# Optimization experiments

Hardware: AMD Instinct MI355X
Metric: run time of the kernel (lower is better)

The kernel has to match this reference:

```python
import jax, jax.numpy as jnp
import numpy as np

TOP_K = 2  # num_experts_per_tok


def setup_inputs() -> dict:
    key = jax.random.key(0)
    k1, k2, k3, k4, k5 = jax.random.split(key, 5)
    T, H, F, E = 2048, 2048, 1024, 8
    hidden_states = jax.random.normal(k1, (T, H), dtype=jnp.float32)
    router_logits = jax.random.normal(k2, (T, E), dtype=jnp.float32)
    s = 1.0 / np.sqrt(H)
    w1 = jax.random.normal(k3, (E, H, F), dtype=jnp.float32) * s  # gate proj
    w3 = jax.random.normal(k4, (E, H, F), dtype=jnp.float32) * s  # up proj
    w2 = jax.random.normal(k5, (E, F, H), dtype=jnp.float32) * (1.0 / np.sqrt(F))  # down proj
    return {"hidden_states": hidden_states, "router_logits": router_logits,
            "w1": w1, "w3": w3, "w2": w2}


def reference(hidden_states, router_logits, w1, w3, w2):
    # Top-K routing: softmax over raw logits, take top-k probs as combine weights
    # (renormalize_topk_logits=False, routed_scaling_factor=None).
    T, E = router_logits.shape
    probs = jax.nn.softmax(router_logits.astype(jnp.float32), axis=-1)  # (T, E)
    topk_w, topk_ids = jax.lax.top_k(probs, TOP_K)                      # (T, K)
    # Scatter combine weights into a dense (T, E) matrix (zeros off top-k).
    combine = jnp.zeros((T, E), dtype=probs.dtype).at[
        jnp.arange(T)[:, None], topk_ids].add(topk_w)                    # (T, E)

    x = hidden_states
    # SwiGLU expert FFN computed per-expert (dense over all tokens, masked by
    # combine weights -> same math as fused dispatch/grouped-GEMM/combine).
    g = jnp.einsum('th,ehf->etf', x, w1)          # (E, T, F) gate
    u = jnp.einsum('th,ehf->etf', x, w3)          # (E, T, F) up
    act = jax.nn.silu(g) * u                      # (E, T, F)
    act = act * combine.T[:, :, None]             # apply combine weight pre-down-proj
    y = jnp.einsum('etf,efh->th', act, w2)        # (T, H) combined over experts
    return y.astype(hidden_states.dtype)
```

## Files before the change

### kernel.cpp

```cpp
#include <hip/hip_runtime.h>
#include <stdint.h>

#define T_TOK 2048
#define HDIM  2048
#define FDIM  1024
#define NEXP  8

#define BM   128
#define BK   64
#define NTHR 256
#define MT_MAX 16
#define BN1  64
#define BN2  128
#define NT1 (FDIM / BN1)
#define NT2 (HDIM / BN2)
#define NK1 (HDIM / BK)
#define NK2 (FDIM / BK)
#define GRID2K (NEXP * MT_MAX * NT2)
#define TILE_E 4096
#define SMEM_BYTES 36864

typedef unsigned short u16;
typedef __attribute__((ext_vector_type(16))) float f32x16;
typedef __attribute__((ext_vector_type(8))) short bf16x8;

__device__ __forceinline__ u16 f2bf(float f) {
  uint32_t u = __float_as_uint(f);
  u += 0x7FFFu + ((u >> 16) & 1u);
  return (u16)(u >> 16);
}

__device__ __forceinline__ uint32_t pack2(float lo, float hi) {
  return (uint32_t)f2bf(lo) | ((uint32_t)f2bf(hi) << 16);
}

__device__ __forceinline__ void glds16(const u16* src, u16* dst) {
  __builtin_amdgcn_global_load_lds(
      (const __attribute__((address_space(1))) uint32_t*)src,
      (__attribute__((address_space(3))) uint32_t*)dst, 16, 0, 0);
}

__global__ void route1_kernel(const float* __restrict__ logits,
                              int* __restrict__ tok_e, float* __restrict__ tok_w,
                              int* __restrict__ counts) {
  __shared__ int lcnt[NEXP];
  const int tid = threadIdx.x;
  const int t = blockIdx.x * 256 + tid;
  if (tid < NEXP) lcnt[tid] = 0;
  __syncthreads();
  float l[NEXP];
#pragma unroll
  for (int e = 0; e < NEXP; ++e) l[e] = logits[t * NEXP + e];
  float m = l[0];
#pragma unroll
  for (int e = 1; e < NEXP; ++e) m = fmaxf(m, l[e]);
  float p[NEXP]; float s = 0.f;
#pragma unroll
  for (int e = 0; e < NEXP; ++e) { p[e] = __expf(l[e] - m); s += p[e]; }
  float inv = 1.f / s;
  int i0 = 0; float p0 = p[0];
#pragma unroll
  for (int e = 1; e < NEXP; ++e) if (p[e] > p0) { p0 = p[e]; i0 = e; }
  int i1 = -1; float p1 = -1.f;
#pragma unroll
  for (int e = 0; e < NEXP; ++e) if (e != i0 && p[e] > p1) { p1 = p[e]; i1 = e; }
  tok_e[t] = i0 | (i1 << 8);
  tok_w[t * 2]     = p0 * inv;
  tok_w[t * 2 + 1] = p1 * inv;
  atomicAdd(&lcnt[i0], 1);
  atomicAdd(&lcnt[i1], 1);
  __syncthreads();
  if (tid < NEXP) atomicAdd(&counts[tid], lcnt[tid]);
}

__global__ void route2_kernel(const int* __restrict__ counts,
                              int* __restrict__ offsets, int* __restrict__ cursor) {
  if (threadIdx.x == 0) {
    int s = 0;
    for (int e = 0; e < NEXP; ++e) { offsets[e] = s; cursor[e] = s; s += counts[e]; }
    offsets[NEXP] = s;
  }
}

__global__ void route3_kernel(const int* __restrict__ tok_e, const float* __restrict__ tok_w,
                              int* __restrict__ cursor,
                              int* __restrict__ token_list, float* __restrict__ slot_w) {
  __shared__ int lcnt[NEXP], lbase[NEXP];
  const int tid = threadIdx.x;
  const int t = blockIdx.x * 256 + tid;
  if (tid < NEXP) lcnt[tid] = 0;
  __syncthreads();
  int ee = tok_e[t];
  int e0 = ee & 255, e1 = ee >> 8;
  int li0 = atomicAdd(&lcnt[e0], 1);
  int li1 = atomicAdd(&lcnt[e1], 1);
  __syncthreads();
  if (tid < NEXP) lbase[tid] = atomicAdd(&cursor[tid], lcnt[tid]);
  __syncthreads();
  int s0 = lbase[e0] + li0;
  int s1 = lbase[e1] + li1;
  token_list[s0] = t; slot_w[s0] = tok_w[t * 2];
  token_list[s1] = t; slot_w[s1] = tok_w[t * 2 + 1];
}

__device__ __forceinline__ void wconv_block(const float* __restrict__ src,
                                            u16* __restrict__ dstb,
                                            int C, int NT, int NKT,
                                            int e, int r0, int c0, uint32_t* L) {
  const int t = threadIdx.x;
  const int p  = t >> 5;
  const int ln = t & 31;
  const float* row0 = src + (size_t)(r0 + 2 * p) * C + c0;
  const float* row1 = row0 + C;
  float4 f0[8], f1[8];
#pragma unroll
  for (int j = 0; j < 8; ++j) f0[j] = *(const float4*)(row0 + j * 128 + ln * 4);
#pragma unroll
  for (int j = 0; j < 8; ++j) f1[j] = *(const float4*)(row1 + j * 128 + ln * 4);
#pragma unroll
  for (int j = 0; j < 8; ++j) {
    int n = j * 128 + ln * 4;
    L[(n + 0) * 9 + p] = pack2(f0[j].x, f1[j].x);
    L[(n + 1) * 9 + p] = pack2(f0[j].y, f1[j].y);
    L[(n + 2) * 9 + p] = pack2(f0[j].z, f1[j].z);
    L[(n + 3) * 9 + p] = pack2(f0[j].w, f1[j].w);
  }
  __syncthreads();
  const int kt = r0 >> 6, kq = (r0 >> 4) & 3;
#pragma unroll
  for (int i = 0; i < 4; ++i) {
    int n = t * 4 + i;
    const uint32_t* a = &L[n * 9];
    uint4 lo = {a[0], a[1], a[2], a[3]};
    uint4 hi = {a[4], a[5], a[6], a[7]};
    int ng = c0 + n;
    int s = (n >> 2) & 1;
    u16* tb = dstb + (((size_t)e * NT + (ng >> 6)) * NKT + kt) * TILE_E
                   + kq * 1024 + (n & 63) * 16;
    *(uint4*)(tb + s * 8)       = lo;
    *(uint4*)(tb + (s ^ 1) * 8) = hi;
  }
}

__global__ __launch_bounds__(256, 3)
void mega1_kernel(const float* __restrict__ w1, const float* __restrict__ w3,
                  u16* __restrict__ w1b, u16* __restrict__ w3b,
                  const float4* __restrict__ x, ushort4* __restrict__ xb,
                  float4* __restrict__ y4) {
  __shared__ __align__(16) uint8_t smem[SMEM_BYTES];
  const int bid = blockIdx.x;
  const int t = threadIdx.x;
  if (bid < 2048) {
    const int m = bid >> 10;
    const int r = bid & 1023;
    const int e = r >> 7;
    const int g = r & 127;
    const size_t msz = (size_t)HDIM * FDIM;
    wconv_block((m ? w3 : w1) + (size_t)e * msz, m ? w3b : w1b,
                FDIM, 16, 32, e, g * 16, 0, (uint32_t*)smem);
  } else if (bid < 2304) {
    int i = (bid - 2048) * 256 + t;
#pragma unroll
    for (int r = 0; r < 16; ++r, i += 65536) {
      float4 v = x[i];
      ushort4 o;
      o.x = f2bf(v.x); o.y = f2bf(v.y); o.z = f2bf(v.z); o.w = f2bf(v.w);
      xb[i] = o;
    }
  } else {
    int i = (bid - 2304) * 256 + t;
    float4 z = {0.f, 0.f, 0.f, 0.f};
#pragma unroll
    for (int r = 0; r < 16; ++r, i += 65536) y4[i] = z;
  }
}

__global__ __launch_bounds__(256, 3)
void mega2_kernel(const float* __restrict__ w2, u16* __restrict__ w2b,
                  const u16* __restrict__ Xb,
                  const u16* __restrict__ w1b, const u16* __restrict__ w3b,
                  const int* __restrict__ token_list,
                  const float* __restrict__ slot_w,
                  const int* __restrict__ counts,
                  const int* __restrict__ offsets,
                  u16* __restrict__ act) {
  __shared__ __align__(16) uint8_t smem[SMEM_BYTES];
  const int bid = blockIdx.x;
  if (bid < 1024) {
    const int e = bid >> 7;
    const int r = bid & 127;
    const int g = r & 63;
    const int half = r >> 6;
    wconv_block(w2 + (size_t)e * HDIM * FDIM, w2b,
                HDIM, 32, 16, e, g * 16, half * 1024, (uint32_t*)smem);
    return;
  }
  const int gb = bid - 1024;
  const int e  = gb >> 8;
  const int mt = (gb >> 4) & 15;
  const int nt = gb & 15;
  const int cnt = counts[e];
  if (mt * BM >= cnt) return;
  const int off = offsets[e];
  const int tid  = threadIdx.x;
  const int lane = tid & 63;
  const int wid  = tid >> 6;
  const int wr = wid >> 1;
  const int wc = wid & 1;

  u16* A_lds  = (u16*)smem;
  u16* B1_lds = (u16*)(smem + 16384);
  u16* B3_lds = (u16*)(smem + 24576);

  const u16* a_src[4];
#pragma unroll
  for (int i = 0; i < 4; ++i) {
    int row = (wid * 4 + i) * 8 + (lane >> 3);
    int mg = mt * BM + row;
    int mc = (mg < cnt) ? mg : (cnt - 1);
    int tok = token_list[off + mc];
    a_src[i] = Xb + (size_t)tok * HDIM + (((lane & 7) ^ (row & 7)) * 8);
  }
  const u16* b1_src[2];
  const u16* b3_src[2];
  {
    size_t tbase = ((size_t)(e * 16 + nt) * 32) * TILE_E;
#pragma unroll
    for (int i = 0; i < 2; ++i) {
      int c = wid * 2 + i;
      b1_src[i] = w1b + tbase + c * 512 + lane * 8;
      b3_src[i] = w3b + tbase + c * 512 + lane * 8;
    }
  }

  f32x16 accg[2] = {};
  f32x16 accu[2] = {};

#pragma unroll
  for (int i = 0; i < 4; ++i) glds16(a_src[i], &A_lds[(wid * 4 + i) * 512]);
#pragma unroll
  for (int i = 0; i < 2; ++i) {
    glds16(b1_src[i], &B1_lds[(wid * 2 + i) * 512]);
    glds16(b3_src[i], &B3_lds[(wid * 2 + i) * 512]);
  }

#pragma unroll 1
  for (int t = 0; t < NK1; ++t) {
    __syncthreads();
    bf16x8 af[2][4], bg[4], bu[4];
#pragma unroll
    for (int m = 0; m < 2; ++m) {
      int R = wr * 64 + m * 32 + (lane & 31);
#pragma unroll
      for (int kk = 0; kk < 4; ++kk) {
        int gl = kk * 2 + (lane >> 5);
        af[m][kk] = *(const bf16x8*)&A_lds[R * BK + ((gl ^ (R & 7)) * 8)];
      }
    }
    {
      int R = wc * 32 + (lane & 31);
      int base = R * 16 + (((lane >> 5) ^ ((R >> 2) & 1)) * 8);
#pragma unroll
      for (int kk = 0; kk < 4; ++kk) {
        bg[kk] = *(const bf16x8*)&B1_lds[base + kk * 1024];
        bu[kk] = *(const bf16x8*)&B3_lds[base + kk * 1024];
      }
    }
    __syncthreads();
    if (t + 1 < NK1) {
      const size_t ks = (size_t)(t + 1) * BK;
      const size_t kb = (size_t)(t + 1) * TILE_E;
#pragma unroll
      for (int i = 0; i < 4; ++i) glds16(a_src[i] + ks, &A_lds[(wid * 4 + i) * 512]);
#pragma unroll
      for (int i = 0; i < 2; ++i) {
        glds16(b1_src[i] + kb, &B1_lds[(wid * 2 + i) * 512]);
        glds16(b3_src[i] + kb, &B3_lds[(wid * 2 + i) * 512]);
      }
    }
#pragma unroll
    for (int m = 0; m < 2; ++m)
#pragma unroll
      for (int kk = 0; kk < 4; ++kk) {
        accg[m] = __builtin_amdgcn_mfma_f32_32x32x16_bf16(af[m][kk], bg[kk], accg[m], 0, 0, 0);
        accu[m] = __builtin_amdgcn_mfma_f32_32x32x16_bf16(af[m][kk], bu[kk], accu[m], 0, 0, 0);
      }
  }

  const int fcol = nt * BN1 + wc * 32 + (lane & 31);
#pragma unroll
  for (int m = 0; m < 2; ++m) {
    int base = mt * BM + wr * 64 + m * 32 + 4 * (lane >> 5);
#pragma unroll
    for (int reg = 0; reg < 16; ++reg) {
      int mg = base + (reg & 3) + 8 * (reg >> 2);
      if (mg < cnt) {
        int slot = off + mg;
        float wgt = slot_w[slot];
        float g = accg[m][reg];
        float u = accu[m][reg];
        float sv = g / (1.f + __expf(-g));
        act[(size_t)slot * FDIM + fcol] = f2bf(sv * u * wgt);
      }
    }
  }
}

__global__ __launch_bounds__(NTHR, 3)
void gemm2_kernel(const u16* __restrict__ act,
                  const u16* __restrict__ w2b,
                  const int* __restrict__ token_list,
                  const int* __restrict__ counts,
                  const int* __restrict__ offsets,
                  float* __restrict__ y) {
  const int bid = blockIdx.x;
  const int e  = bid >> 8;
  const int mt = (bid >> 4) & 15;
  const int nt = bid & 15;
  const int cnt = counts[e];
  if (mt * BM >= cnt) return;
  const int off = offsets[e];
  const int tid  = threadIdx.x;
  const int lane = tid & 63;
  const int wid  = tid >> 6;
  const int wr = wid >> 1;
  const int wc = wid & 1;

  __shared__ u16 A_lds[BM * BK];
  __shared__ u16 B_lds[BN2 * BK];

  const u16* a_src[4];
  const u16* b_src[4];
#pragma unroll
  for (int i = 0; i < 4; ++i) {
    int row = (wid * 4 + i) * 8 + (lane >> 3);
    int mg = mt * BM + row;
    int mc = (mg < cnt) ? mg : (cnt - 1);
    a_src[i] = act + (size_t)(off + mc) * FDIM + (((lane & 7) ^ (row & 7)) * 8);
    int c = wid * 4 + i;
    size_t tbase = ((size_t)(e * 32 + nt * 2 + (c >> 3)) * 16) * TILE_E;
    b_src[i] = w2b + tbase + (c & 7) * 512 + lane * 8;
  }

  f32x16 acc[2][2] = {};

#pragma unroll
  for (int i = 0; i < 4; ++i) {
    glds16(a_src[i], &A_lds[(wid * 4 + i) * 512]);
    glds16(b_src[i], &B_lds[(wid * 4 + i) * 512]);
  }

#pragma unroll 1
  for (int t = 0; t < NK2; ++t) {
    __syncthreads();
    bf16x8 af[2][4], bb[2][4];
#pragma unroll
    for (int m = 0; m < 2; ++m) {
      int R = wr * 64 + m * 32 + (lane & 31);
#pragma unroll
      for (int kk = 0; kk < 4; ++kk) {
        int gl = kk * 2 + (lane >> 5);
        af[m][kk] = *(const bf16x8*)&A_lds[R * BK + ((gl ^ (R & 7)) * 8)];
      }
    }
#pragma unroll
    for (int n = 0; n < 2; ++n) {
      int R = wc * 64 + n * 32 + (lane & 31);
      int base = (R >> 6) * TILE_E + (R & 63) * 16 + (((lane >> 5) ^ ((R >> 2) & 1)) * 8);
#pragma unroll
      for (int kk = 0; kk < 4; ++kk)
        bb[n][kk] = *(const bf16x8*)&B_lds[base + kk * 1024];
    }
    __syncthreads();
    if (t + 1 < NK2) {
      const size_t ks = (size_t)(t + 1) * BK;
      const size_t kb = (size_t)(t + 1) * TILE_E;
#pragma unroll
      for (int i = 0; i < 4; ++i) {
        glds16(a_src[i] + ks, &A_lds[(wid * 4 + i) * 512]);
        glds16(b_src[i] + kb, &B_lds[(wid * 4 + i) * 512]);
      }
    }
#pragma unroll
    for (int kk = 0; kk < 4; ++kk)
#pragma unroll
      for (int m = 0; m < 2; ++m)
#pragma unroll
        for (int n = 0; n < 2; ++n)
          acc[m][n] = __builtin_amdgcn_mfma_f32_32x32x16_bf16(af[m][kk], bb[n][kk], acc[m][n], 0, 0, 0);
  }

#pragma unroll
  for (int m = 0; m < 2; ++m) {
    int base = mt * BM + wr * 64 + m * 32 + 4 * (lane >> 5);
#pragma unroll
    for (int reg = 0; reg < 16; ++reg) {
      int mg = base + (reg & 3) + 8 * (reg >> 2);
      if (mg < cnt) {
        int slot = off + mg;
        int tok = token_list[slot];
#pragma unroll
        for (int n = 0; n < 2; ++n) {
          int hcol = nt * BN2 + wc * 64 + n * 32 + (lane & 31);
          unsafeAtomicAdd(y + (size_t)tok * HDIM + hcol, acc[m][n][reg]);
        }
      }
    }
  }
}

extern "C" void kernel_launch(void* const* d_in, const int* in_sizes, int n_in,
                              void* d_out, int out_size, void* d_ws, size_t ws_size,
                              hipStream_t stream) {
  (void)in_sizes; (void)n_in; (void)out_size; (void)ws_size;
  const float* hs     = (const float*)d_in[0];
  const float* logits = (const float*)d_in[1];
  const float* w1     = (const float*)d_in[2];
  const float* w3     = (const float*)d_in[3];
  const float* w2     = (const float*)d_in[4];
  float* y = (float*)d_out;

  uint8_t* ws = (uint8_t*)d_ws;
  int*   token_list = (int*)(ws);
  float* slot_w     = (float*)(ws + (16 << 10));
  int*   counts     = (int*)(ws + (32 << 10));
  int*   offsets    = (int*)(ws + (32 << 10) + 128);
  int*   cursor     = (int*)(ws + (32 << 10) + 256);
  int*   tok_e      = (int*)(ws + (33 << 10));
  float* tok_w      = (float*)(ws + (42 << 10));
  const size_t MB = 1 << 20;
  u16*   Xb  = (u16*)(ws + (64 << 10));
  u16*   act = (u16*)(ws + (64 << 10) + 8 * MB);
  u16*   w1b = (u16*)(ws + (64 << 10) + 16 * MB);
  u16*   w3b = (u16*)(ws + (64 << 10) + 48 * MB);
  u16*   w2b = (u16*)(ws + (64 << 10) + 80 * MB);

  hipMemsetAsync(counts, 0, NEXP * sizeof(int), stream);
  route1_kernel<<<T_TOK / 256, 256, 0, stream>>>(logits, tok_e, tok_w, counts);
  route2_kernel<<<1, 64, 0, stream>>>(counts, offsets, cursor);
  route3_kernel<<<T_TOK / 256, 256, 0, stream>>>(tok_e, tok_w, cursor, token_list, slot_w);
  mega1_kernel<<<2560, 256, 0, stream>>>(w1, w3, w1b, w3b,
                                         (const float4*)hs, (ushort4*)Xb, (float4*)y);
  mega2_kernel<<<3072, 256, 0, stream>>>(w2, w2b, Xb, w1b, w3b,
                                         token_list, slot_w, counts, offsets, act);
  gemm2_kernel<<<GRID2K, NTHR, 0, stream>>>(act, w2b, token_list, counts, offsets, y);
}
```

Before: 181.9 us.

## Double-buffer LDS tiles in both expert GEMM kernels

Gives the gate/up and down-projection GEMMs two LDS buffers each, so the next K tile's global-to-LDS load is issued into the other buffer while MFMAs run on the current one. This cuts each K step from two barriers to one. The cost is doubled shared memory (64 KB per block), which lowers the occupancy hint from 3 to 2 blocks per CU and reduces latency hiding across blocks.

```diff
diff --git a/kernel.cpp b/kernel.cpp
--- a/kernel.cpp
+++ b/kernel.cpp
@@ -18,7 +18,7 @@
 #define NK2 (FDIM / BK)
 #define GRID2K (NEXP * MT_MAX * NT2)
 #define TILE_E 4096
-#define SMEM_BYTES 36864
+#define SMEM2 65536
 
 typedef unsigned short u16;
 typedef __attribute__((ext_vector_type(16))) float f32x16;
@@ -147,7 +147,7 @@
                   u16* __restrict__ w1b, u16* __restrict__ w3b,
                   const float4* __restrict__ x, ushort4* __restrict__ xb,
                   float4* __restrict__ y4) {
-  __shared__ __align__(16) uint8_t smem[SMEM_BYTES];
+  __shared__ __align__(16) uint8_t smem[36864];
   const int bid = blockIdx.x;
   const int t = threadIdx.x;
   if (bid < 2048) {
@@ -175,7 +175,7 @@
   }
 }
 
-__global__ __launch_bounds__(256, 3)
+__global__ __launch_bounds__(256, 2)
 void mega2_kernel(const float* __restrict__ w2, u16* __restrict__ w2b,
                   const u16* __restrict__ Xb,
                   const u16* __restrict__ w1b, const u16* __restrict__ w3b,
@@ -184,7 +184,7 @@
                   const int* __restrict__ counts,
                   const int* __restrict__ offsets,
                   u16* __restrict__ act) {
-  __shared__ __align__(16) uint8_t smem[SMEM_BYTES];
+  __shared__ __align__(16) uint8_t smem[SMEM2];
   const int bid = blockIdx.x;
   if (bid < 1024) {
     const int e = bid >> 7;
@@ -208,9 +208,12 @@
   const int wr = wid >> 1;
   const int wc = wid & 1;
 
-  u16* A_lds  = (u16*)smem;
-  u16* B1_lds = (u16*)(smem + 16384);
-  u16* B3_lds = (u16*)(smem + 24576);
+  u16* A0  = (u16*)smem;
+  u16* A1  = (u16*)(smem + 16384);
+  u16* B10 = (u16*)(smem + 32768);
+  u16* B30 = (u16*)(smem + 40960);
+  u16* B11 = (u16*)(smem + 49152);
+  u16* B31 = (u16*)(smem + 57344);
 
   const u16* a_src[4];
 #pragma unroll
@@ -235,57 +238,63 @@
 
   f32x16 accg[2] = {};
   f32x16 accu[2] = {};
-
-#pragma unroll
-  for (int i = 0; i < 4; ++i) glds16(a_src[i], &A_lds[(wid * 4 + i) * 512]);
-#pragma unroll
-  for (int i = 0; i < 2; ++i) {
-    glds16(b1_src[i], &B1_lds[(wid * 2 + i) * 512]);
-    glds16(b3_src[i], &B3_lds[(wid * 2 + i) * 512]);
-  }
+  bf16x8 af[2][4], bg[4], bu[4];
+
+#define STAGE1(Ab, B1b, B3b, T)                                          \
+  { const size_t ks = (size_t)(T) * BK;                                  \
+    const size_t kb = (size_t)(T) * TILE_E;                              \
+    _Pragma("unroll")                                                    \
+    for (int i = 0; i < 4; ++i) glds16(a_src[i] + ks, &Ab[(wid * 4 + i) * 512]); \
+    _Pragma("unroll")                                                    \
+    for (int i = 0; i < 2; ++i) {                                        \
+      glds16(b1_src[i] + kb, &B1b[(wid * 2 + i) * 512]);                 \
+      glds16(b3_src[i] + kb, &B3b[(wid * 2 + i) * 512]);                 \
+    } }
+
+#define FRAGS1(Ab, B1b, B3b)                                             \
+  { _Pragma("unroll")                                                    \
+    for (int m = 0; m < 2; ++m) {                                        \
+      int R = wr * 64 + m * 32 + (lane & 31);                            \
+      _Pragma("unroll")                                                  \
+      for (int kk = 0; kk < 4; ++kk) {                                   \
+        int gl = kk * 2 + (lane >> 5);                                   \
+        af[m][kk] = *(const bf16x8*)&Ab[R * BK + ((gl ^ (R & 7)) * 8)];  \
+      }                                                                  \
+    }                                                                    \
+    { int R = wc * 32 + (lane & 31);                                     \
+      int base = R * 16 + (((lane >> 5) ^ ((R >> 2) & 1)) * 8);          \
+      _Pragma("unroll")                                                  \
+      for (int kk = 0; kk < 4; ++kk) {                                   \
+        bg[kk] = *(const bf16x8*)&B1b[base + kk * 1024];                 \
+        bu[kk] = *(const bf16x8*)&B3b[base + kk * 1024];                 \
+      } } }
+
+#define MFMA1                                                            \
+  { _Pragma("unroll")                                                    \
+    for (int m = 0; m < 2; ++m)                                          \
+      _Pragma("unroll")                                                  \
+      for (int kk = 0; kk < 4; ++kk) {                                   \
+        accg[m] = __builtin_amdgcn_mfma_f32_32x32x16_bf16(af[m][kk], bg[kk], accg[m], 0, 0, 0); \
+        accu[m] = __builtin_amdgcn_mfma_f32_32x32x16_bf16(af[m][kk], bu[kk], accu[m], 0, 0, 0); \
+      } }
+
+  STAGE1(A0, B10, B30, 0);
+  __syncthreads();
 
 #pragma unroll 1
-  for (int t = 0; t < NK1; ++t) {
+  for (int t = 0; t < NK1; t += 2) {
+    FRAGS1(A0, B10, B30);
+    STAGE1(A1, B11, B31, t + 1);
+    MFMA1;
     __syncthreads();
-    bf16x8 af[2][4], bg[4], bu[4];
-#pragma unroll
-    for (int m = 0; m < 2; ++m) {
-      int R = wr * 64 + m * 32 + (lane & 31);
-#pragma unroll
-      for (int kk = 0; kk < 4; ++kk) {
-        int gl = kk * 2 + (lane >> 5);
-        af[m][kk] = *(const bf16x8*)&A_lds[R * BK + ((gl ^ (R & 7)) * 8)];
-      }
-    }
-    {
-      int R = wc * 32 + (lane & 31);
-      int base = R * 16 + (((lane >> 5) ^ ((R >> 2) & 1)) * 8);
-#pragma unroll
-      for (int kk = 0; kk < 4; ++kk) {
-        bg[kk] = *(const bf16x8*)&B1_lds[base + kk * 1024];
-        bu[kk] = *(const bf16x8*)&B3_lds[base + kk * 1024];
-      }
-    }
+    FRAGS1(A1, B11, B31);
+    if (t + 2 < NK1) STAGE1(A0, B10, B30, t + 2);
+    MFMA1;
     __syncthreads();
-    if (t + 1 < NK1) {
-      const size_t ks = (size_t)(t + 1) * BK;
-      const size_t kb = (size_t)(t + 1) * TILE_E;
-#pragma unroll
-      for (int i = 0; i < 4; ++i) glds16(a_src[i] + ks, &A_lds[(wid * 4 + i) * 512]);
-#pragma unroll
-      for (int i = 0; i < 2; ++i) {
-        glds16(b1_src[i] + kb, &B1_lds[(wid * 2 + i) * 512]);
-        glds16(b3_src[i] + kb, &B3_lds[(wid * 2 + i) * 512]);
-      }
-    }
-#pragma unroll
-    for (int m = 0; m < 2; ++m)
-#pragma unroll
-      for (int kk = 0; kk < 4; ++kk) {
-        accg[m] = __builtin_amdgcn_mfma_f32_32x32x16_bf16(af[m][kk], bg[kk], accg[m], 0, 0, 0);
-        accu[m] = __builtin_amdgcn_mfma_f32_32x32x16_bf16(af[m][kk], bu[kk], accu[m], 0, 0, 0);
-      }
-  }
+  }
+#undef STAGE1
+#undef FRAGS1
+#undef MFMA1
 
   const int fcol = nt * BN1 + wc * 32 + (lane & 31);
 #pragma unroll
@@ -306,7 +315,7 @@
   }
 }
 
-__global__ __launch_bounds__(NTHR, 3)
+__global__ __launch_bounds__(NTHR, 2)
 void gemm2_kernel(const u16* __restrict__ act,
                   const u16* __restrict__ w2b,
                   const int* __restrict__ token_list,
@@ -326,8 +335,10 @@
   const int wr = wid >> 1;
   const int wc = wid & 1;
 
-  __shared__ u16 A_lds[BM * BK];
-  __shared__ u16 B_lds[BN2 * BK];
+  __shared__ u16 A0[BM * BK];
+  __shared__ u16 A1[BM * BK];
+  __shared__ u16 B0[BN2 * BK];
+  __shared__ u16 B1[BN2 * BK];
 
   const u16* a_src[4];
   const u16* b_src[4];
@@ -343,52 +354,62 @@
   }
 
   f32x16 acc[2][2] = {};
-
-#pragma unroll
-  for (int i = 0; i < 4; ++i) {
-    glds16(a_src[i], &A_lds[(wid * 4 + i) * 512]);
-    glds16(b_src[i], &B_lds[(wid * 4 + i) * 512]);
-  }
+  bf16x8 af[2][4], bb[2][4];
+
+#define STAGE2(Ab, Bb, T)                                                \
+  { const size_t ks = (size_t)(T) * BK;                                  \
+    const size_t kb = (size_t)(T) * TILE_E;                              \
+    _Pragma("unroll")                                                    \
+    for (int i = 0; i < 4; ++i) {                                        \
+      glds16(a_src[i] + ks, &Ab[(wid * 4 + i) * 512]);                   \
+      glds16(b_src[i] + kb, &Bb[(wid * 4 + i) * 512]);                   \
+    } }
+
+#define FRAGS2(Ab, Bb)                                                   \
+  { _Pragma("unroll")                                                    \
+    for (int m = 0; m < 2; ++m) {                                        \
+      int R = wr * 64 + m * 32 + (lane & 31);                            \
+      _Pragma("unroll")                                                  \
+      for (int kk = 0; kk < 4; ++kk) {                                   \
+        int gl = kk * 2 + (lane >> 5);                                   \
+        af[m][kk] = *(const bf16x8*)&Ab[R * BK + ((gl ^ (R & 7)) * 8)];  \
+      }                                                                  \
+    }                                                                    \
+    _Pragma("unroll")                                                    \
+    for (int n = 0; n < 2; ++n) {                                        \
+      int R = wc * 64 + n * 32 + (lane & 31);                            \
+      int base = (R >> 6) * TILE_E + (R & 63) * 16 + (((lane >> 5) ^ ((R >> 2) & 1)) * 8); \
+      _Pragma("unroll")                                                  \
+      for (int kk = 0; kk < 4; ++kk)                                     \
+        bb[n][kk] = *(const bf16x8*)&Bb[base + kk * 1024];               \
+    } }
+
+#define MFMA2                                                            \
+  { _Pragma("unroll")                                                    \
+    for (int kk = 0; kk < 4; ++kk)                                       \
+      _Pragma("unroll")                                                  \
+      for (int m = 0; m < 2; ++m)                                        \
+        _Pragma("unroll")                                                \
+        for (int n = 0; n < 2; ++n)                                      \
+          acc[m][n] = __builtin_amdgcn_mfma_f32_32x32x16_bf16(af[m][kk], bb[n][kk], acc[m][n], 0, 0, 0); }
+
+  STAGE2(A0, B0, 0);
+  __syncthreads();
 
 #pragma unroll 1
-  for (int t = 0; t < NK2; ++t) {
+  for (int t = 0; t < NK2; t += 2) {
+    FRAGS2(A0, B0);
+    STAGE2(A1, B1, t + 1);
+    MFMA2;
     __syncthreads();
-    bf16x8 af[2][4], bb[2][4];
-#pragma unroll
-    for (int m = 0; m < 2; ++m) {
-      int R = wr * 64 + m * 32 + (lane & 31);
-#pragma unroll
-      for (int kk = 0; kk < 4; ++kk) {
-        int gl = kk * 2 + (lane >> 5);
-        af[m][kk] = *(const bf16x8*)&A_lds[R * BK + ((gl ^ (R & 7)) * 8)];
-      }
-    }
-#pragma unroll
-    for (int n = 0; n < 2; ++n) {
-      int R = wc * 64 + n * 32 + (lane & 31);
-      int base = (R >> 6) * TILE_E + (R & 63) * 16 + (((lane >> 5) ^ ((R >> 2) & 1)) * 8);
-#pragma unroll
-      for (int kk = 0; kk < 4; ++kk)
-        bb[n][kk] = *(const bf16x8*)&B_lds[base + kk * 1024];
-    }
+    FRAGS2(A1, B1);
+    if (t + 2 < NK2) STAGE2(A0, B0, t + 2);
+    MFMA2;
     __syncthreads();
-    if (t + 1 < NK2) {
-      const size_t ks = (size_t)(t + 1) * BK;
-      const size_t kb = (size_t)(t + 1) * TILE_E;
-#pragma unroll
-      for (int i = 0; i < 4; ++i) {
-        glds16(a_src[i] + ks, &A_lds[(wid * 4 + i) * 512]);
-        glds16(b_src[i] + kb, &B_lds[(wid * 4 + i) * 512]);
-      }
-    }
-#pragma unroll
-    for (int kk = 0; kk < 4; ++kk)
-#pragma unroll
-      for (int m = 0; m < 2; ++m)
-#pragma unroll
-        for (int n = 0; n < 2; ++n)
-          acc[m][n] = __builtin_amdgcn_mfma_f32_32x32x16_bf16(af[m][kk], bb[n][kk], acc[m][n], 0, 0, 0);
-  }
+  }
+#undef STAGE2
+#undef FRAGS2
+#undef MFMA2
 
 #pragma unroll
   for (int m = 0; m < 2; ++m) {
```

After: 214.3 us. 1.18x slower.

## Fuse w1/w3 fp32-to-bf16 conversion into the gate/up GEMM B-tile loads

Applied to the files above, without the earlier changes.

Drops the separate pass that converted w1 and w3 to tiled bf16 in a workspace. The gate/up GEMM now loads fp32 weights directly, converts them in registers and writes swizzled bf16 into LDS, interleaved between two halves of the MFMA loop. This removes one full write and re-read of 64 MB of bf16 weights. In exchange, each M-tile block re-reads fp32 weights (twice the bytes per load), and conversion uses VALU and register time inside the GEMM's critical loop.

```diff
diff --git a/kernel.cpp b/kernel.cpp
--- a/kernel.cpp
+++ b/kernel.cpp
@@ -18,7 +18,6 @@
 #define NK2 (FDIM / BK)
 #define GRID2K (NEXP * MT_MAX * NT2)
 #define TILE_E 4096
-#define SMEM_BYTES 36864
 
 typedef unsigned short u16;
 typedef __attribute__((ext_vector_type(16))) float f32x16;
@@ -101,6 +100,28 @@
   int s1 = lbase[e1] + li1;
   token_list[s0] = t; slot_w[s0] = tok_w[t * 2];
   token_list[s1] = t; slot_w[s1] = tok_w[t * 2 + 1];
+}
+
+__global__ __launch_bounds__(256)
+void mega1_kernel(const float4* __restrict__ x, ushort4* __restrict__ xb,
+                  float4* __restrict__ y4) {
+  const int bid = blockIdx.x;
+  const int t = threadIdx.x;
+  if (bid < 256) {
+    int i = bid * 256 + t;
+#pragma unroll
+    for (int r = 0; r < 16; ++r, i += 65536) {
+      float4 v = x[i];
+      ushort4 o;
+      o.x = f2bf(v.x); o.y = f2bf(v.y); o.z = f2bf(v.z); o.w = f2bf(v.w);
+      xb[i] = o;
+    }
+  } else {
+    int i = (bid - 256) * 256 + t;
+    float4 z = {0.f, 0.f, 0.f, 0.f};
+#pragma unroll
+    for (int r = 0; r < 16; ++r, i += 65536) y4[i] = z;
+  }
 }
 
 __device__ __forceinline__ void wconv_block(const float* __restrict__ src,
@@ -143,48 +164,15 @@
 }
 
 __global__ __launch_bounds__(256, 3)
-void mega1_kernel(const float* __restrict__ w1, const float* __restrict__ w3,
-                  u16* __restrict__ w1b, u16* __restrict__ w3b,
-                  const float4* __restrict__ x, ushort4* __restrict__ xb,
-                  float4* __restrict__ y4) {
-  __shared__ __align__(16) uint8_t smem[SMEM_BYTES];
-  const int bid = blockIdx.x;
-  const int t = threadIdx.x;
-  if (bid < 2048) {
-    const int m = bid >> 10;
-    const int r = bid & 1023;
-    const int e = r >> 7;
-    const int g = r & 127;
-    const size_t msz = (size_t)HDIM * FDIM;
-    wconv_block((m ? w3 : w1) + (size_t)e * msz, m ? w3b : w1b,
-                FDIM, 16, 32, e, g * 16, 0, (uint32_t*)smem);
-  } else if (bid < 2304) {
-    int i = (bid - 2048) * 256 + t;
-#pragma unroll
-    for (int r = 0; r < 16; ++r, i += 65536) {
-      float4 v = x[i];
-      ushort4 o;
-      o.x = f2bf(v.x); o.y = f2bf(v.y); o.z = f2bf(v.z); o.w = f2bf(v.w);
-      xb[i] = o;
-    }
-  } else {
-    int i = (bid - 2304) * 256 + t;
-    float4 z = {0.f, 0.f, 0.f, 0.f};
-#pragma unroll
-    for (int r = 0; r < 16; ++r, i += 65536) y4[i] = z;
-  }
-}
-
-__global__ __launch_bounds__(256, 3)
 void mega2_kernel(const float* __restrict__ w2, u16* __restrict__ w2b,
                   const u16* __restrict__ Xb,
-                  const u16* __restrict__ w1b, const u16* __restrict__ w3b,
+                  const float* __restrict__ w1, const float* __restrict__ w3,
                   const int* __restrict__ token_list,
                   const float* __restrict__ slot_w,
                   const int* __restrict__ counts,
                   const int* __restrict__ offsets,
                   u16* __restrict__ act) {
-  __shared__ __align__(16) uint8_t smem[SMEM_BYTES];
+  __shared__ __align__(16) uint8_t smem[36864];
   const int bid = blockIdx.x;
   if (bid < 1024) {
     const int e = bid >> 7;
@@ -211,6 +199,8 @@
   u16* A_lds  = (u16*)smem;
   u16* B1_lds = (u16*)(smem + 16384);
   u16* B3_lds = (u16*)(smem + 24576);
+  uint32_t* B1u = (uint32_t*)B1_lds;
+  uint32_t* B3u = (uint32_t*)B3_lds;
 
   const u16* a_src[4];
 #pragma unroll
@@ -221,33 +211,42 @@
     int tok = token_list[off + mc];
     a_src[i] = Xb + (size_t)tok * HDIM + (((lane & 7) ^ (row & 7)) * 8);
   }
-  const u16* b1_src[2];
-  const u16* b3_src[2];
-  {
-    size_t tbase = ((size_t)(e * 16 + nt) * 32) * TILE_E;
-#pragma unroll
-    for (int i = 0; i < 2; ++i) {
-      int c = wid * 2 + i;
-      b1_src[i] = w1b + tbase + c * 512 + lane * 8;
-      b3_src[i] = w3b + tbase + c * 512 + lane * 8;
-    }
-  }
+
+  const int p  = tid >> 3;
+  const int cg = tid & 7;
+  const int g  = p >> 2;
+  const int po = p & 3;
+  const float* pw1 = w1 + (size_t)e * HDIM * FDIM + (size_t)(2 * p) * FDIM + nt * BN1 + cg * 8;
+  const float* pw3 = w3 + (size_t)e * HDIM * FDIM + (size_t)(2 * p) * FDIM + nt * BN1 + cg * 8;
 
   f32x16 accg[2] = {};
   f32x16 accu[2] = {};
-
+  bf16x8 af[2][4], bg[4], bu[4];
+  float4 xa, xb_, xc, xd;
+
+#define LOADBP(PW, T) { const float* q = (PW) + (size_t)(T) * BK * FDIM;       \
+    xa = *(const float4*)(q);        xb_ = *(const float4*)(q + 4);            \
+    xc = *(const float4*)(q + FDIM); xd  = *(const float4*)(q + FDIM + 4); }
+
+#define CVTWP(Bu) {                                                            \
+    Bu[(cg*8+0)*32 + ((g ^ cg ^ 0) * 4) + po] = pack2(xa.x, xc.x);             \
+    Bu[(cg*8+1)*32 + ((g ^ cg ^ 1) * 4) + po] = pack2(xa.y, xc.y);             \
+    Bu[(cg*8+2)*32 + ((g ^ cg ^ 2) * 4) + po] = pack2(xa.z, xc.z);             \
+    Bu[(cg*8+3)*32 + ((g ^ cg ^ 3) * 4) + po] = pack2(xa.w, xc.w);             \
+    Bu[(cg*8+4)*32 + ((g ^ cg ^ 4) * 4) + po] = pack2(xb_.x, xd.x);            \
+    Bu[(cg*8+5)*32 + ((g ^ cg ^ 5) * 4) + po] = pack2(xb_.y, xd.y);            \
+    Bu[(cg*8+6)*32 + ((g ^ cg ^ 6) * 4) + po] = pack2(xb_.z, xd.z);            \
+    Bu[(cg*8+7)*32 + ((g ^ cg ^ 7) * 4) + po] = pack2(xb_.w, xd.w); }
+
+  LOADBP(pw1, 0); CVTWP(B1u);
+  LOADBP(pw3, 0); CVTWP(B3u);
 #pragma unroll
   for (int i = 0; i < 4; ++i) glds16(a_src[i], &A_lds[(wid * 4 + i) * 512]);
-#pragma unroll
-  for (int i = 0; i < 2; ++i) {
-    glds16(b1_src[i], &B1_lds[(wid * 2 + i) * 512]);
-    glds16(b3_src[i], &B3_lds[(wid * 2 + i) * 512]);
-  }
 
 #pragma unroll 1
   for (int t = 0; t < NK1; ++t) {
     __syncthreads();
-    bf16x8 af[2][4], bg[4], bu[4];
+    if (t + 1 < NK1) LOADBP(pw1, t + 1);
 #pragma unroll
     for (int m = 0; m < 2; ++m) {
       int R = wr * 64 + m * 32 + (lane & 31);
@@ -258,34 +257,43 @@
       }
     }
     {
-      int R = wc * 32 + (lane & 31);
-      int base = R * 16 + (((lane >> 5) ^ ((R >> 2) & 1)) * 8);
+      int n = wc * 32 + (lane & 31);
+      int S = ((n >> 3) ^ n) & 7;
 #pragma unroll
       for (int kk = 0; kk < 4; ++kk) {
-        bg[kk] = *(const bf16x8*)&B1_lds[base + kk * 1024];
-        bu[kk] = *(const bf16x8*)&B3_lds[base + kk * 1024];
+        int gl = kk * 2 + (lane >> 5);
+        bg[kk] = *(const bf16x8*)&B1_lds[n * 64 + ((gl ^ S) * 8)];
+        bu[kk] = *(const bf16x8*)&B3_lds[n * 64 + ((gl ^ S) * 8)];
       }
     }
     __syncthreads();
     if (t + 1 < NK1) {
       const size_t ks = (size_t)(t + 1) * BK;
-      const size_t kb = (size_t)(t + 1) * TILE_E;
 #pragma unroll
       for (int i = 0; i < 4; ++i) glds16(a_src[i] + ks, &A_lds[(wid * 4 + i) * 512]);
-#pragma unroll
-      for (int i = 0; i < 2; ++i) {
-        glds16(b1_src[i] + kb, &B1_lds[(wid * 2 + i) * 512]);
-        glds16(b3_src[i] + kb, &B3_lds[(wid * 2 + i) * 512]);
-      }
     }
 #pragma unroll
     for (int m = 0; m < 2; ++m)
 #pragma unroll
-      for (int kk = 0; kk < 4; ++kk) {
+      for (int kk = 0; kk < 2; ++kk) {
         accg[m] = __builtin_amdgcn_mfma_f32_32x32x16_bf16(af[m][kk], bg[kk], accg[m], 0, 0, 0);
         accu[m] = __builtin_amdgcn_mfma_f32_32x32x16_bf16(af[m][kk], bu[kk], accu[m], 0, 0, 0);
       }
-  }
+    if (t + 1 < NK1) {
+      CVTWP(B1u);
+      LOADBP(pw3, t + 1);
+    }
+#pragma unroll
+    for (int m = 0; m < 2; ++m)
+#pragma unroll
+      for (int kk = 2; kk < 4; ++kk) {
+        accg[m] = __builtin_amdgcn_mfma_f32_32x32x16_bf16(af[m][kk], bg[kk], accg[m], 0, 0, 0);
+        accu[m] = __builtin_amdgcn_mfma_f32_32x32x16_bf16(af[m][kk], bu[kk], accu[m], 0, 0, 0);
+      }
+    if (t + 1 < NK1) CVTWP(B3u);
+  }
+#undef LOADBP
+#undef CVTWP
 
   const int fcol = nt * BN1 + wc * 32 + (lane & 31);
 #pragma unroll
@@ -297,10 +305,10 @@
       if (mg < cnt) {
         int slot = off + mg;
         float wgt = slot_w[slot];
-        float g = accg[m][reg];
-        float u = accu[m][reg];
-        float sv = g / (1.f + __expf(-g));
-        act[(size_t)slot * FDIM + fcol] = f2bf(sv * u * wgt);
+        float gv = accg[m][reg];
+        float uv = accu[m][reg];
+        float sv = gv / (1.f + __expf(-gv));
+        act[(size_t)slot * FDIM + fcol] = f2bf(sv * uv * wgt);
       }
     }
   }
@@ -431,17 +439,14 @@
   const size_t MB = 1 << 20;
   u16*   Xb  = (u16*)(ws + (64 << 10));
   u16*   act = (u16*)(ws + (64 << 10) + 8 * MB);
-  u16*   w1b = (u16*)(ws + (64 << 10) + 16 * MB);
-  u16*   w3b = (u16*)(ws + (64 << 10) + 48 * MB);
-  u16*   w2b = (u16*)(ws + (64 << 10) + 80 * MB);
+  u16*   w2b = (u16*)(ws + (64 << 10) + 16 * MB);
 
   hipMemsetAsync(counts, 0, NEXP * sizeof(int), stream);
   route1_kernel<<<T_TOK / 256, 256, 0, stream>>>(logits, tok_e, tok_w, counts);
   route2_kernel<<<1, 64, 0, stream>>>(counts, offsets, cursor);
   route3_kernel<<<T_TOK / 256, 256, 0, stream>>>(tok_e, tok_w, cursor, token_list, slot_w);
-  mega1_kernel<<<2560, 256, 0, stream>>>(w1, w3, w1b, w3b,
-                                         (const float4*)hs, (ushort4*)Xb, (float4*)y);
-  mega2_kernel<<<3072, 256, 0, stream>>>(w2, w2b, Xb, w1b, w3b,
+  mega1_kernel<<<512, 256, 0, stream>>>((const float4*)hs, (ushort4*)Xb, (float4*)y);
+  mega2_kernel<<<3072, 256, 0, stream>>>(w2, w2b, Xb, w1, w3,
                                          token_list, slot_w, counts, offsets, act);
   gemm2_kernel<<<GRID2K, NTHR, 0, stream>>>(act, w2b, token_list, counts, offsets, y);
 }
```

Measured after the change: 198.5 us. +9.1%, slower.
